# Performance work log

Hardware: AMD Instinct MI355X
Metric: run time of the kernel (lower is better)

## Reference

```python
import jax, jax.numpy as jnp
import numpy as np

PI = float(np.pi)


def _layernorm(x, g, b, eps=1e-5):
    mu = jnp.mean(x, axis=-1, keepdims=True)
    var = jnp.var(x, axis=-1, keepdims=True)
    return (x - mu) * jax.lax.rsqrt(var + eps) * g + b


def setup_inputs() -> dict:
    key = jax.random.key(0)
    B, L, D, P = 4, 2048, 256, 32
    ks = jax.random.split(key, 16)

    def lin_w(k, fi, fo):
        return (jax.random.normal(k, (fi, fo), dtype=jnp.float32) / np.sqrt(fi)).astype(jnp.float32)

    inp = {
        'x': jax.random.normal(ks[0], (B, L, D), dtype=jnp.float32),
        'pos_phases': jax.random.normal(ks[1], (L, P), dtype=jnp.float32) * PI,
        'w_mem1v': lin_w(ks[2], D, P), 'b_mem1v': jnp.zeros((P,), jnp.float32),
        'w_mem1o': lin_w(ks[3], P, D), 'b_mem1o': jnp.zeros((D,), jnp.float32),
        'w_off': lin_w(ks[4], D + P, P), 'b_off': jnp.zeros((P,), jnp.float32),
        'w_key': lin_w(ks[5], D, P), 'b_key': jnp.zeros((P,), jnp.float32),
        'w_val': lin_w(ks[6], D, D), 'b_val': jnp.zeros((D,), jnp.float32),
        'w_sk1': lin_w(ks[7], 2 * D, D), 'b_sk1': jnp.zeros((D,), jnp.float32),
        'w_sk2': lin_w(ks[8], D, P), 'b_sk2': jnp.zeros((P,), jnp.float32),
        'w_gate': lin_w(ks[9], D, 1), 'b_gate': jnp.zeros((1,), jnp.float32),
        'ln_g': jnp.ones((D,), jnp.float32), 'ln_b': jnp.zeros((D,), jnp.float32),
        'w_out': lin_w(ks[10], D, D), 'b_out': jnp.zeros((D,), jnp.float32),
    }
    return inp


def reference(x, pos_phases, w_mem1v, b_mem1v, w_mem1o, b_mem1o, w_off, b_off,
              w_key, b_key, w_val, b_val, w_sk1, b_sk1, w_sk2, b_sk2,
              w_gate, b_gate, ln_g, ln_b, w_out, b_out):
    B, L, D = x.shape
    P = pos_phases.shape[-1]

    pos_cos = jnp.cos(pos_phases)  # [L,P]
    pos_sin = jnp.sin(pos_phases)

    # Memory 1: flat [B,L,P] phasor cumulative memory
    v1 = x @ w_mem1v + b_mem1v                       # [B,L,P]
    mem1_cos = jnp.cumsum(pos_cos[None] * v1, axis=1)
    mem1_sin = jnp.cumsum(pos_sin[None] * v1, axis=1)

    offset_input = jnp.concatenate([x, jnp.broadcast_to(pos_phases[None], (B, L, P))], axis=-1)
    offset = jnp.tanh(offset_input @ w_off + b_off) * PI
    oc, os = jnp.cos(offset), jnp.sin(offset)
    query_cos = pos_cos[None] * oc - pos_sin[None] * os
    query_sin = pos_sin[None] * oc + pos_cos[None] * os
    pos_ret = (mem1_cos * query_cos + mem1_sin * query_sin) / np.sqrt(P)
    pos_out = pos_ret @ w_mem1o + b_mem1o            # [B,L,D]

    # Memory 2: full [B,L,P,D] phasor KV cumulative memory
    key_phases = jnp.tanh(x @ w_key + b_key) * PI    # [B,L,P]
    key_cos, key_sin = jnp.cos(key_phases), jnp.sin(key_phases)
    values = x @ w_val + b_val                       # [B,L,D]
    store_gate = jax.nn.sigmoid(x @ w_gate + b_gate) # [B,L,1]

    positions = jnp.arange(1, L + 1, dtype=x.dtype)[None, :, None]
    context_avg = jnp.cumsum(x, axis=1) / positions
    h = jax.nn.gelu(jnp.concatenate([x, context_avg], axis=-1) @ w_sk1 + b_sk1, approximate=False)
    storage_phases = jnp.tanh(h @ w_sk2 + b_sk2) * PI  # [B,L,P]

    gated_v = values * store_gate                    # [B,L,D]
    kv_mem_cos = jnp.cumsum(jnp.cos(storage_phases)[..., None] * gated_v[:, :, None, :], axis=1)  # [B,L,P,D]
    kv_mem_sin = jnp.cumsum(jnp.sin(storage_phases)[..., None] * gated_v[:, :, None, :], axis=1)

    gate_cumsum = jnp.clip(jnp.cumsum(store_gate, axis=1), 1.0, None)  # [B,L,1]
    kv_retrieved = jnp.einsum('blpd,blp->bld', kv_mem_cos, key_cos) + \
                   jnp.einsum('blpd,blp->bld', kv_mem_sin, key_sin)
    kv_retrieved = kv_retrieved / (jnp.sqrt(gate_cumsum) * np.sqrt(P))

    combined = pos_out + kv_retrieved
    return x + _layernorm(combined, ln_g, ln_b) @ w_out + b_out
```

## Files before the change

kernel.cpp:

```cpp
#include <hip/hip_runtime.h>
#include <hip/hip_bf16.h>

constexpr int B_ = 4;
constexpr int L_ = 2048;
constexpr int D_ = 256;
constexpr int P_ = 32;
constexpr int CL = 32;
constexpr int NC = L_ / CL;

#define PI_F 3.14159265358979323846f
#define INV_SQRT_P 0.17677669529663687f

typedef __attribute__((ext_vector_type(8))) short short8_t;
typedef __attribute__((ext_vector_type(4))) float floatx4;

static __device__ inline short f2bf(float f) {
  unsigned int u;
  __builtin_memcpy(&u, &f, 4);
  unsigned int r = (u + 0x7fffu + ((u >> 16) & 1u)) >> 16;
  return (short)r;
}
static __device__ inline float bf2f(short s) {
  unsigned int u = ((unsigned int)(unsigned short)s) << 16;
  float f;
  __builtin_memcpy(&f, &u, 4);
  return f;
}

__global__ void wprep(const float* __restrict__ x, const float* __restrict__ pos,
                      const float* __restrict__ w_val, const float* __restrict__ w_mem1v,
                      const float* __restrict__ w_off, const float* __restrict__ b_off,
                      const float* __restrict__ w_key, const float* __restrict__ w_gate,
                      const float* __restrict__ w_sk1, const float* __restrict__ w_out,
                      const float* __restrict__ w_sk2, const float* __restrict__ w_mem1o,
                      short* __restrict__ WA, short* __restrict__ W1,
                      short* __restrict__ WO, short* __restrict__ W2T,
                      short* __restrict__ W1OT,
                      short* __restrict__ xbf, float* __restrict__ poff,
                      float* __restrict__ ctxsum) {
  __shared__ float2 psum[2][128];
  int blk = blockIdx.x, tid = threadIdx.x;
  if (blk < 384) {
    int idx = blk * 256 + tid;
    int n = idx >> 8, k = idx & 255;
    float v;
    if (n < 256) v = w_val[k * 256 + n];
    else if (n < 288) v = w_mem1v[k * 32 + (n - 256)];
    else if (n < 320) v = w_off[k * 32 + (n - 288)];
    else if (n < 352) v = w_key[k * 32 + (n - 320)];
    else if (n == 352) v = w_gate[k];
    else v = 0.f;
    WA[idx] = f2bf(v);
  } else if (blk < 896) {
    int idx = (blk - 384) * 256 + tid;
    int n = idx >> 9, k = idx & 511;
    W1[idx] = f2bf(w_sk1[k * 256 + n]);
  } else if (blk < 1152) {
    int idx = (blk - 896) * 256 + tid;
    int n = idx >> 8, k = idx & 255;
    WO[idx] = f2bf(w_out[k * 256 + n]);
  } else if (blk < 1184) {
    int idx = (blk - 1152) * 256 + tid;
    int p = idx >> 8, k = idx & 255;
    W2T[idx] = f2bf(w_sk2[k * 32 + p]);
  } else if (blk < 1216) {
    int idx = (blk - 1184) * 256 + tid;
    int d = idx >> 5, p = idx & 31;
    W1OT[idx] = f2bf(w_mem1o[p * 256 + d]);
  } else if (blk < 1472) {
    int idx = (blk - 1216) * 256 + tid;
    int l = idx >> 5, p = idx & 31;
    float a = b_off[p];
#pragma unroll 8
    for (int j = 0; j < 32; ++j) a += pos[l * 32 + j] * w_off[(256 + j) * 32 + p];
    poff[idx] = a;
  } else {
    int c2 = blk - 1472;
    int b = c2 >> 6, ch = c2 & 63;
    int d2 = (tid & 127) * 2, h = tid >> 7;
    int tokb = b * L_ + ch * 32 + h * 16;
    float2 xv[16];
#pragma unroll
    for (int i = 0; i < 16; ++i)
      xv[i] = *(const float2*)&x[(tokb + i) * 256 + d2];
    float2 s = {0.f, 0.f};
#pragma unroll
    for (int i = 0; i < 16; ++i) { s.x += xv[i].x; s.y += xv[i].y; }
#pragma unroll
    for (int i = 0; i < 16; ++i) {
      short2 o;
      o.x = f2bf(xv[i].x);
      o.y = f2bf(xv[i].y);
      *(short2*)&xbf[(tokb + i) * 256 + d2] = o;
    }
    psum[h][tid & 127] = s;
    __syncthreads();
    if (h == 0) {
      float2 o = psum[1][tid & 127];
      float2 tot = {s.x + o.x, s.y + o.y};
      *(float2*)&ctxsum[c2 * 256 + d2] = tot;
    }
  }
}

__global__ __launch_bounds__(768, 6) void gemmA3(const short* __restrict__ xbf,
                                                 const short* __restrict__ WA,
                                                 const float* __restrict__ pos,
                                                 const float* __restrict__ poff,
                                                 const float* __restrict__ b_mem1v,
                                                 const float* __restrict__ b_key,
                                                 const float* __restrict__ b_gate,
                                                 const float* __restrict__ b_val,
                                                 float* __restrict__ m1cT,
                                                 float* __restrict__ m1sT,
                                                 float* __restrict__ qc,
                                                 float* __restrict__ qs,
                                                 short* __restrict__ K2bf,
                                                 short* __restrict__ gvT,
                                                 float* __restrict__ sg,
                                                 float* __restrict__ ctxsum) {
  __shared__ float YL[16][132];
  __shared__ float gsh[16];
  int tid = threadIdx.x;
  int bc = blockIdx.x;
  if (bc >= 512) {
    if (tid < 256) {
      int b = bc - 512;
      int base = b * 64 * 256 + tid;
      float run = 0.f;
      for (int c0 = 0; c0 < 64; c0 += 8) {
        float v[8];
#pragma unroll
        for (int j = 0; j < 8; ++j) v[j] = ctxsum[base + (c0 + j) * 256];
#pragma unroll
        for (int j = 0; j < 8; ++j) {
          ctxsum[base + (c0 + j) * 256] = run;
          run += v[j];
        }
      }
    }
    return;
  }
  int lane = tid & 63, w = tid >> 6;
  int ml = lane & 15, quad = lane >> 4, kq = quad * 8;
  int bc32 = bc >> 1, half = bc & 1;
  int tok0 = bc * 16;
  float posv = 0.f, poffv = 0.f;
  if (tid < 512) {
    int t = tid >> 5, p = tid & 31;
    int l = (tok0 + t) & (L_ - 1);
    posv = pos[l * 32 + p];
    poffv = poff[l * 32 + p];
  }
  floatx4 acc[2] = {};
  const short* A0p = &xbf[(tok0 + ml) * 256 + kq];
  const short* Bp = &WA[(w * 32 + ml) * 256 + kq];
#pragma unroll
  for (int ks = 0; ks < 8; ++ks) {
    short8_t a0 = *(const short8_t*)(A0p + ks * 32);
#pragma unroll
    for (int nt = 0; nt < 2; ++nt) {
      short8_t b = *(const short8_t*)(Bp + nt * 16 * 256 + ks * 32);
      acc[nt] = __builtin_amdgcn_mfma_f32_16x16x32_bf16(a0, b, acc[nt], 0, 0, 0);
    }
  }
  if (w >= 8) {
#pragma unroll
    for (int nt = 0; nt < 2; ++nt) {
      int col = (w - 8) * 32 + nt * 16 + ml;
#pragma unroll
      for (int r = 0; r < 4; ++r)
        YL[quad * 4 + r][col] = acc[nt][r];
    }
  }
  __syncthreads();
  if (tid < 512) {
    int t = tid >> 5, p = tid & 31;
    int tok = tok0 + t, l = tok & (L_ - 1);
    int b = tok >> 11;
    float v1 = YL[t][p] + b_mem1v[p];
    float pc = cosf(posv), ps = sinf(posv);
    int idxT = (b * 32 + p) * L_ + l;
    m1cT[idxT] = pc * v1;
    m1sT[idxT] = ps * v1;
    float off = tanhf(YL[t][32 + p] + poffv) * PI_F;
    float oc = cosf(off), os = sinf(off);
    int gidx = tok * 32 + p;
    qc[gidx] = pc * oc - ps * os;
    qs[gidx] = ps * oc + pc * os;
    float kp = tanhf(YL[t][64 + p] + b_key[p]) * PI_F;
    K2bf[tok * 64 + p] = f2bf(cosf(kp));
    K2bf[tok * 64 + 32 + p] = f2bf(sinf(kp));
    if (p == 0) {
      float g = 1.f / (1.f + expf(-(YL[t][96] + b_gate[0])));
      sg[tok] = g;
      gsh[t] = g;
    }
  }
  __syncthreads();
  if (w < 8) {
#pragma unroll
    for (int nt = 0; nt < 2; ++nt) {
      int d = w * 32 + nt * 16 + ml;
      float bv = b_val[d];
      int t0 = quad * 4;
      short4 o;
      o.x = f2bf((acc[nt][0] + bv) * gsh[t0 + 0]);
      o.y = f2bf((acc[nt][1] + bv) * gsh[t0 + 1]);
      o.z = f2bf((acc[nt][2] + bv) * gsh[t0 + 2]);
      o.w = f2bf((acc[nt][3] + bv) * gsh[t0 + 3]);
      *(short4*)&gvT[(bc32 * 256 + d) * 32 + half * 16 + t0] = o;
    }
  }
}

union __align__(16) CDMem {
  short As[32][520];
  struct { short HS[32][280]; short SPL[64][40]; } h;
};
__global__ __launch_bounds__(1024, 4) void gemmCD(const short* __restrict__ xbf,
                                                  const float* __restrict__ x,
                                                  const float* __restrict__ ctxsum,
                                                  const short* __restrict__ W1,
                                                  const float* __restrict__ b_sk1,
                                                  const short* __restrict__ W2T,
                                                  const float* __restrict__ b_sk2,
                                                  const short* __restrict__ gvT,
                                                  short* __restrict__ SPbf,
                                                  short* __restrict__ UT) {
  __shared__ CDMem sm;
  __shared__ float stmp[4][256];
  int tid = threadIdx.x;
  int bc = blockIdx.x;
  int tok0 = bc * 32;
  int bI = bc >> 6, ch = bc & 63;
  int lane = tid & 63, w = tid >> 6;
  int ml = lane & 15, quad = lane >> 4, kq = quad * 8;
  short8_t bgv = *(const short8_t*)&gvT[(bc * 256 + w * 16 + ml) * 32 + kq];
  {
    int row = tid >> 5, c8 = tid & 31;
    *(short8_t*)&sm.As[row][c8 * 8] =
        *(const short8_t*)&xbf[(tok0 + row) * 256 + c8 * 8];
  }
  {
    int d = tid & 255, qh = tid >> 8;
    float cp = ctxsum[(bI * 64 + ch) * 256 + d];
    float xv[8];
    int xb = (tok0 + qh * 8) * 256 + d;
#pragma unroll
    for (int i = 0; i < 8; ++i) xv[i] = x[xb + i * 256];
    float p = 0.f;
#pragma unroll
    for (int i = 0; i < 8; ++i) p += xv[i];
    stmp[qh][d] = p;
    __syncthreads();
    float run = cp;
    for (int j = 0; j < qh; ++j) run += stmp[j][d];
    int l0 = ch * 32 + qh * 8;
#pragma unroll
    for (int i = 0; i < 8; ++i) {
      run += xv[i];
      sm.As[qh * 8 + i][256 + d] = f2bf(run / (float)(l0 + i + 1));
    }
  }
  __syncthreads();
  int n0w = w * 16;
  floatx4 acc[2] = {};
#pragma unroll
  for (int kt = 0; kt < 16; ++kt) {
    short8_t a0 = *(short8_t*)&sm.As[ml][kt * 32 + kq];
    short8_t a1 = *(short8_t*)&sm.As[16 + ml][kt * 32 + kq];
    short8_t b0 = *(const short8_t*)&W1[(n0w + ml) * 512 + kt * 32 + kq];
    acc[0] = __builtin_amdgcn_mfma_f32_16x16x32_bf16(a0, b0, acc[0], 0, 0, 0);
    acc[1] = __builtin_amdgcn_mfma_f32_16x16x32_bf16(a1, b0, acc[1], 0, 0, 0);
  }
  short hv[2][4];
  {
    float bv = b_sk1[n0w + ml];
#pragma unroll
    for (int mt = 0; mt < 2; ++mt)
#pragma unroll
      for (int r = 0; r < 4; ++r) {
        float v = acc[mt][r] + bv;
        float g = 0.5f * v * (1.f + erff(v * 0.70710678118654752f));
        hv[mt][r] = f2bf(g);
      }
  }
  __syncthreads();
#pragma unroll
  for (int mt = 0; mt < 2; ++mt)
#pragma unroll
    for (int r = 0; r < 4; ++r)
      sm.h.HS[mt * 16 + quad * 4 + r][n0w + ml] = hv[mt][r];
  __syncthreads();
  if (w < 4) {
    int th = w & 1, ph = w >> 1;
    floatx4 pacc = {};
#pragma unroll
    for (int s = 0; s < 8; ++s) {
      short8_t a = *(short8_t*)&sm.h.HS[th * 16 + ml][s * 32 + kq];
      short8_t b0 = *(const short8_t*)&W2T[(ph * 16 + ml) * 256 + s * 32 + kq];
      pacc = __builtin_amdgcn_mfma_f32_16x16x32_bf16(a, b0, pacc, 0, 0, 0);
    }
    int p = ph * 16 + ml;
    float bs = b_sk2[p];
#pragma unroll
    for (int r = 0; r < 4; ++r) {
      int tl = th * 16 + quad * 4 + r;
      int tok = tok0 + tl;
      float sp = tanhf(pacc[r] + bs) * PI_F;
      short c = f2bf(cosf(sp)), s2 = f2bf(sinf(sp));
      sm.h.SPL[p][tl] = c;
      sm.h.SPL[32 + p][tl] = s2;
      SPbf[tok * 64 + p] = c;
      SPbf[tok * 64 + 32 + p] = s2;
    }
  }
  __syncthreads();
  short8_t a[4];
#pragma unroll
  for (int mt = 0; mt < 4; ++mt) a[mt] = *(short8_t*)&sm.h.SPL[mt * 16 + ml][kq];
  floatx4 acc3[4] = {};
#pragma unroll
  for (int mt = 0; mt < 4; ++mt)
    acc3[mt] = __builtin_amdgcn_mfma_f32_16x16x32_bf16(a[mt], bgv, acc3[mt], 0, 0, 0);
#pragma unroll
  for (int mt = 0; mt < 4; ++mt) {
    int d = w * 16 + ml;
    short4 o;
    o.x = f2bf(acc3[mt][0]);
    o.y = f2bf(acc3[mt][1]);
    o.z = f2bf(acc3[mt][2]);
    o.w = f2bf(acc3[mt][3]);
    *(short4*)&UT[(bc * 256 + d) * 64 + mt * 16 + quad * 4] = o;
  }
}

__global__ void scanE(float* __restrict__ m1cT, float* __restrict__ m1sT,
                      float* __restrict__ sg, short* __restrict__ UT) {
  __shared__ float wsum[4];
  __shared__ float stot[4][64];
  int blk = blockIdx.x;
  int tid = threadIdx.x;
  if (blk >= 260) {
    int eb = blk - 260;
    int w = tid >> 6, lane = tid & 63;
    int pi = eb * 64 + lane;
    int q = pi & 63;
    int d = (pi >> 6) & 255;
    int b = pi >> 14;
    const int cs = 256 * 64;
    int base = ((b * NC) * 256 + d) * 64 + q;
    short v[16];
#pragma unroll
    for (int c = 0; c < 16; ++c) v[c] = UT[base + (w * 16 + c) * cs];
    float tot = 0.f;
#pragma unroll
    for (int c = 0; c < 16; ++c) tot += bf2f(v[c]);
    stot[w][lane] = tot;
    __syncthreads();
    float run = 0.f;
    for (int ww = 0; ww < w; ++ww) run += stot[ww][lane];
#pragma unroll
    for (int c = 0; c < 16; ++c) {
      UT[base + (w * 16 + c) * cs] = f2bf(run);
      run += bf2f(v[c]);
    }
    return;
  }
  int lane = tid & 63, w = tid >> 6;
  float* arr;
  int base;
  if (blk < 256) {
    arr = (blk < 128) ? m1cT : m1sT;
    base = (blk & 127) * L_;
  } else {
    arr = sg;
    base = (blk - 256) * L_;
  }
  int sbase = base + w * 512;
  float v[8];
#pragma unroll
  for (int i = 0; i < 8; ++i) v[i] = arr[sbase + i * 64 + lane];
  float carry = 0.f;
#pragma unroll
  for (int i = 0; i < 8; ++i) {
    float vv = v[i];
#pragma unroll
    for (int off = 1; off < 64; off <<= 1) {
      float n = __shfl_up(vv, off, 64);
      if (lane >= off) vv += n;
    }
    vv += carry;
    v[i] = vv;
    carry = __shfl(vv, 63, 64);
  }
  if (lane == 0) wsum[w] = carry;
  __syncthreads();
  float off = 0.f;
  for (int ww = 0; ww < w; ++ww) off += wsum[ww];
#pragma unroll
  for (int i = 0; i < 8; ++i) arr[sbase + i * 64 + lane] = v[i] + off;
}

struct __align__(16) FGMem {
  short SL[32][40];
  short PR[32][40];
  float CMB[32][260];
  short CBN[32][280];
  float LG[256], LB[256];
  float scl[32], mu_s[32], rs_s[32];
};
__global__ __launch_bounds__(1024, 4) void fgOut(const short* __restrict__ UT,
                                                 const short* __restrict__ SPbf,
                                                 const short* __restrict__ K2bf,
                                                 const short* __restrict__ gvT,
                                                 const float* __restrict__ sgc,
                                                 const float* __restrict__ m1cT,
                                                 const float* __restrict__ m1sT,
                                                 const float* __restrict__ qc,
                                                 const float* __restrict__ qs,
                                                 const short* __restrict__ W1OT,
                                                 const float* __restrict__ b_mem1o,
                                                 const float* __restrict__ ln_g,
                                                 const float* __restrict__ ln_b,
                                                 const short* __restrict__ WO,
                                                 const float* __restrict__ b_out,
                                                 const float* __restrict__ x,
                                                 float* __restrict__ out) {
  __shared__ FGMem sm;
  int tid5 = threadIdx.x;
  int bc = blockIdx.x;
  int lbase = bc * CL;
  int bb = bc >> 6, lloc = (bc & 63) * 32;
  int lane = tid5 & 63, w = tid5 >> 6;
  int ml = lane & 15, quad = lane >> 4, kq = quad * 8;
  int d0 = w * 16;
  short8_t ub0 = *(const short8_t*)&UT[(bc * 256 + d0 + ml) * 64 + kq];
  short8_t ub1 = *(const short8_t*)&UT[(bc * 256 + d0 + ml) * 64 + 32 + kq];
  short8_t gvb = *(const short8_t*)&gvT[(bc * 256 + d0 + ml) * 32 + kq];
  short8_t w1b = *(const short8_t*)&W1OT[(d0 + ml) * 32 + kq];
  const float4* x4 = (const float4*)&x[lbase * 256];
  float4 xp0 = x4[tid5];
  float4 xp1 = x4[tid5 + 1024];
  if (tid5 < 32) sm.scl[tid5] = rsqrtf(fmaxf(sgc[lbase + tid5], 1.f)) * INV_SQRT_P;
  if (tid5 >= 256 && tid5 < 512) {
    int d = tid5 - 256;
    sm.LG[d] = ln_g[d];
    sm.LB[d] = ln_b[d];
  }
  short8_t ka0 = *(const short8_t*)&K2bf[(lbase + ml) * 64 + kq];
  short8_t ka1 = *(const short8_t*)&K2bf[(lbase + 16 + ml) * 64 + kq];
  short8_t kb0 = *(const short8_t*)&K2bf[(lbase + ml) * 64 + 32 + kq];
  short8_t kb1 = *(const short8_t*)&K2bf[(lbase + 16 + ml) * 64 + 32 + kq];
  if (w == 0) {
    floatx4 sacc[2][2] = {};
#pragma unroll
    for (int ks2 = 0; ks2 < 2; ++ks2) {
      short8_t a0 = (ks2 == 0) ? ka0 : kb0;
      short8_t a1 = (ks2 == 0) ? ka1 : kb1;
      short8_t b0 = *(const short8_t*)&SPbf[(lbase + ml) * 64 + ks2 * 32 + kq];
      short8_t b1 = *(const short8_t*)&SPbf[(lbase + 16 + ml) * 64 + ks2 * 32 + kq];
      sacc[0][0] = __builtin_amdgcn_mfma_f32_16x16x32_bf16(a0, b0, sacc[0][0], 0, 0, 0);
      sacc[0][1] = __builtin_amdgcn_mfma_f32_16x16x32_bf16(a0, b1, sacc[0][1], 0, 0, 0);
      sacc[1][0] = __builtin_amdgcn_mfma_f32_16x16x32_bf16(a1, b0, sacc[1][0], 0, 0, 0);
      sacc[1][1] = __builtin_amdgcn_mfma_f32_16x16x32_bf16(a1, b1, sacc[1][1], 0, 0, 0);
    }
#pragma unroll
    for (int mt = 0; mt < 2; ++mt)
#pragma unroll
      for (int nt = 0; nt < 2; ++nt)
#pragma unroll
        for (int r = 0; r < 4; ++r) {
          int trow = mt * 16 + quad * 4 + r;
          int scol = nt * 16 + ml;
          float v = (scol <= trow) ? sacc[mt][nt][r] : 0.f;
          sm.SL[trow][scol] = f2bf(v);
        }
  } else {
    int t7 = tid5 - 64;
    for (int i = t7; i < 1024; i += 960) {
      int pp = i >> 5, t = i & 31;
      int gT = (bb * 32 + pp) * L_ + lloc + t;
      int g = (lbase + t) * 32 + pp;
      sm.PR[t][pp] = f2bf((m1cT[gT] * qc[g] + m1sT[gT] * qs[g]) * INV_SQRT_P);
    }
  }
  __syncthreads();
  floatx4 acc[2] = {};
  acc[0] = __builtin_amdgcn_mfma_f32_16x16x32_bf16(ka0, ub0, acc[0], 0, 0, 0);
  acc[1] = __builtin_amdgcn_mfma_f32_16x16x32_bf16(ka1, ub0, acc[1], 0, 0, 0);
  acc[0] = __builtin_amdgcn_mfma_f32_16x16x32_bf16(kb0, ub1, acc[0], 0, 0, 0);
  acc[1] = __builtin_amdgcn_mfma_f32_16x16x32_bf16(kb1, ub1, acc[1], 0, 0, 0);
  {
    short8_t a0 = *(short8_t*)&sm.SL[ml][kq];
    short8_t a1 = *(short8_t*)&sm.SL[16 + ml][kq];
    acc[0] = __builtin_amdgcn_mfma_f32_16x16x32_bf16(a0, gvb, acc[0], 0, 0, 0);
    acc[1] = __builtin_amdgcn_mfma_f32_16x16x32_bf16(a1, gvb, acc[1], 0, 0, 0);
  }
  floatx4 macc[2] = {};
  {
    short8_t a0 = *(short8_t*)&sm.PR[ml][kq];
    short8_t a1 = *(short8_t*)&sm.PR[16 + ml][kq];
    macc[0] = __builtin_amdgcn_mfma_f32_16x16x32_bf16(a0, w1b, macc[0], 0, 0, 0);
    macc[1] = __builtin_amdgcn_mfma_f32_16x16x32_bf16(a1, w1b, macc[1], 0, 0, 0);
  }
  {
    int d = d0 + ml;
    float bm = b_mem1o[d];
#pragma unroll
    for (int mt = 0; mt < 2; ++mt)
#pragma unroll
      for (int r = 0; r < 4; ++r) {
        int t = mt * 16 + quad * 4 + r;
        sm.CMB[t][d] = acc[mt][r] * sm.scl[t] + macc[mt][r] + bm;
      }
  }
  __syncthreads();
  {
    int t = tid5 >> 5, g = tid5 & 31;
    float s = 0.f, s2 = 0.f;
#pragma unroll
    for (int j = 0; j < 8; ++j) {
      float v = sm.CMB[t][g + j * 32];
      s += v;
      s2 += v * v;
    }
#pragma unroll
    for (int m = 1; m < 32; m <<= 1) {
      s += __shfl_xor(s, m, 64);
      s2 += __shfl_xor(s2, m, 64);
    }
    if (g == 0) {
      float mu = s / (float)D_;
      float var = s2 / (float)D_ - mu * mu;
      sm.mu_s[t] = mu;
      sm.rs_s[t] = rsqrtf(var + 1e-5f);
    }
  }
  __syncthreads();
#pragma unroll
  for (int it = 0; it < 8; ++it) {
    int i = it * 1024 + tid5;
    int t = i >> 8, d = i & 255;
    sm.CBN[t][d] = f2bf((sm.CMB[t][d] - sm.mu_s[t]) * sm.rs_s[t] * sm.LG[d] + sm.LB[d]);
  }
  __syncthreads();
  floatx4 acc2[2] = {};
#pragma unroll
  for (int kt = 0; kt < 8; ++kt) {
    short8_t a0 = *(short8_t*)&sm.CBN[ml][kt * 32 + kq];
    short8_t a1 = *(short8_t*)&sm.CBN[16 + ml][kt * 32 + kq];
    short8_t b = *(const short8_t*)&WO[(d0 + ml) * 256 + kt * 32 + kq];
    acc2[0] = __builtin_amdgcn_mfma_f32_16x16x32_bf16(a0, b, acc2[0], 0, 0, 0);
    acc2[1] = __builtin_amdgcn_mfma_f32_16x16x32_bf16(a1, b, acc2[1], 0, 0, 0);
  }
  {
    int n = d0 + ml;
    float bv = b_out[n];
#pragma unroll
    for (int mt = 0; mt < 2; ++mt)
#pragma unroll
      for (int r = 0; r < 4; ++r) {
        int t = mt * 16 + quad * 4 + r;
        sm.CMB[t][n] = acc2[mt][r] + bv;
      }
  }
  __syncthreads();
  {
    float4* o4 = (float4*)&out[lbase * 256];
#pragma unroll
    for (int k = 0; k < 2; ++k) {
      int idx4 = tid5 + k * 1024;
      int t = idx4 >> 6, dd = (idx4 & 63) * 4;
      float4 xp = (k == 0) ? xp0 : xp1;
      float4 o;
      o.x = xp.x + sm.CMB[t][dd + 0];
      o.y = xp.y + sm.CMB[t][dd + 1];
      o.z = xp.z + sm.CMB[t][dd + 2];
      o.w = xp.w + sm.CMB[t][dd + 3];
      o4[idx4] = o;
    }
  }
}

extern "C" void kernel_launch(void* const* d_in, const int* in_sizes, int n_in,
                              void* d_out, int out_size, void* d_ws, size_t ws_size,
                              hipStream_t stream) {
  const float* x = (const float*)d_in[0];
  const float* pos = (const float*)d_in[1];
  const float* w_mem1v = (const float*)d_in[2];
  const float* b_mem1v = (const float*)d_in[3];
  const float* w_mem1o = (const float*)d_in[4];
  const float* b_mem1o = (const float*)d_in[5];
  const float* w_off = (const float*)d_in[6];
  const float* b_off = (const float*)d_in[7];
  const float* w_key = (const float*)d_in[8];
  const float* b_key = (const float*)d_in[9];
  const float* w_val = (const float*)d_in[10];
  const float* b_val = (const float*)d_in[11];
  const float* w_sk1 = (const float*)d_in[12];
  const float* b_sk1 = (const float*)d_in[13];
  const float* w_sk2 = (const float*)d_in[14];
  const float* b_sk2 = (const float*)d_in[15];
  const float* w_gate = (const float*)d_in[16];
  const float* b_gate = (const float*)d_in[17];
  const float* ln_g = (const float*)d_in[18];
  const float* ln_b = (const float*)d_in[19];
  const float* w_out = (const float*)d_in[20];
  const float* b_out = (const float*)d_in[21];
  float* out = (float*)d_out;
  float* ws = (float*)d_ws;

  const int BLP = B_ * L_ * P_;
  const int BLD = B_ * L_ * D_;
  float* m1cT = ws;
  float* m1sT = m1cT + BLP;
  float* qc = m1sT + BLP;
  float* qs = qc + BLP;
  float* sg = qs + BLP;
  float* poff = sg + B_ * L_;
  float* ctxsum = poff + L_ * P_;
  short* UT = (short*)(ctxsum + B_ * 64 * 256);
  short* xbf = UT + (size_t)B_ * NC * 256 * 64;
  short* ctxbf = xbf + BLD;
  short* hs = ctxbf + BLD;
  short* gvT = hs + BLD;
  short* K2bf = gvT + BLD;
  short* SPbf = K2bf + B_ * L_ * 64;
  short* WA = SPbf + B_ * L_ * 64;
  short* W1 = WA + 384 * 256;
  short* WO = W1 + 256 * 512;
  short* W2T = WO + 256 * 256;
  short* W1OT = W2T + 32 * 256;

  wprep<<<1728, 256, 0, stream>>>(x, pos, w_val, w_mem1v, w_off, b_off, w_key, w_gate,
                                  w_sk1, w_out, w_sk2, w_mem1o, WA, W1, WO, W2T, W1OT,
                                  xbf, poff, ctxsum);
  gemmA3<<<516, 768, 0, stream>>>(xbf, WA, pos, poff, b_mem1v, b_key, b_gate, b_val,
                                  m1cT, m1sT, qc, qs, K2bf, gvT, sg, ctxsum);
  gemmCD<<<256, 1024, 0, stream>>>(xbf, x, ctxsum, W1, b_sk1, W2T, b_sk2, gvT, SPbf, UT);
  scanE<<<1284, 256, 0, stream>>>(m1cT, m1sT, sg, UT);
  fgOut<<<256, 1024, 0, stream>>>(UT, SPbf, K2bf, gvT, sg, m1cT, m1sT, qc, qs,
                                  W1OT, b_mem1o, ln_g, ln_b, WO, b_out, x, out);
}
```

Measured before the change: 160.7 us.

## Split gemmCD and fgOut into two 512-thread blocks per chunk

gemmCD now launches two 512-thread blocks per 32-token chunk. Each block recomputes the shared sk1/sk2 stage redundantly, and the final value-projection output is split across the d halves. fgOut is split by token halves (16 tokens per block) with 32 output columns per wave. The aim is to double the number of blocks on the 256-CU part so the GPU is filled better, at the cost of redundant GEMM work in gemmCD and repeated loads in fgOut.

```diff
diff --git a/kernel.cpp b/kernel.cpp
--- a/kernel.cpp
+++ b/kernel.cpp
@@ -218,80 +218,89 @@
   short As[32][520];
   struct { short HS[32][280]; short SPL[64][40]; } h;
 };
-__global__ __launch_bounds__(1024, 4) void gemmCD(const short* __restrict__ xbf,
-                                                  const float* __restrict__ x,
-                                                  const float* __restrict__ ctxsum,
-                                                  const short* __restrict__ W1,
-                                                  const float* __restrict__ b_sk1,
-                                                  const short* __restrict__ W2T,
-                                                  const float* __restrict__ b_sk2,
-                                                  const short* __restrict__ gvT,
-                                                  short* __restrict__ SPbf,
-                                                  short* __restrict__ UT) {
+__global__ __launch_bounds__(512, 4) void gemmCD(const short* __restrict__ xbf,
+                                                 const float* __restrict__ x,
+                                                 const float* __restrict__ ctxsum,
+                                                 const short* __restrict__ W1,
+                                                 const float* __restrict__ b_sk1,
+                                                 const short* __restrict__ W2T,
+                                                 const float* __restrict__ b_sk2,
+                                                 const short* __restrict__ gvT,
+                                                 short* __restrict__ SPbf,
+                                                 short* __restrict__ UT) {
   __shared__ CDMem sm;
-  __shared__ float stmp[4][256];
+  __shared__ float stmp[256];
   int tid = threadIdx.x;
-  int bc = blockIdx.x;
-  int tok0 = bc * 32;
-  int bI = bc >> 6, ch = bc & 63;
+  int cn = blockIdx.x >> 1, dh = blockIdx.x & 1;
+  int tok0 = cn * 32;
+  int bI = cn >> 6, ch = cn & 63;
   int lane = tid & 63, w = tid >> 6;
   int ml = lane & 15, quad = lane >> 4, kq = quad * 8;
-  short8_t bgv = *(const short8_t*)&gvT[(bc * 256 + w * 16 + ml) * 32 + kq];
-  {
-    int row = tid >> 5, c8 = tid & 31;
+  short8_t bgv = *(const short8_t*)&gvT[(cn * 256 + dh * 128 + w * 16 + ml) * 32 + kq];
+#pragma unroll
+  for (int pass = 0; pass < 2; ++pass) {
+    int idx = pass * 512 + tid;
+    int row = idx >> 5, c8 = idx & 31;
     *(short8_t*)&sm.As[row][c8 * 8] =
         *(const short8_t*)&xbf[(tok0 + row) * 256 + c8 * 8];
   }
   {
     int d = tid & 255, qh = tid >> 8;
     float cp = ctxsum[(bI * 64 + ch) * 256 + d];
-    float xv[8];
-    int xb = (tok0 + qh * 8) * 256 + d;
-#pragma unroll
-    for (int i = 0; i < 8; ++i) xv[i] = x[xb + i * 256];
-    float p = 0.f;
-#pragma unroll
-    for (int i = 0; i < 8; ++i) p += xv[i];
-    stmp[qh][d] = p;
+    float xv[16];
+    int xb = (tok0 + qh * 16) * 256 + d;
+#pragma unroll
+    for (int i = 0; i < 16; ++i) xv[i] = x[xb + i * 256];
+    if (qh == 0) {
+      float p = 0.f;
+#pragma unroll
+      for (int i = 0; i < 16; ++i) p += xv[i];
+      stmp[d] = p;
+    }
     __syncthreads();
-    float run = cp;
-    for (int j = 0; j < qh; ++j) run += stmp[j][d];
-    int l0 = ch * 32 + qh * 8;
-#pragma unroll
-    for (int i = 0; i < 8; ++i) {
+    float run = cp + (qh ? stmp[d] : 0.f);
+    int l0 = ch * 32 + qh * 16;
+#pragma unroll
+    for (int i = 0; i < 16; ++i) {
       run += xv[i];
-      sm.As[qh * 8 + i][256 + d] = f2bf(run / (float)(l0 + i + 1));
-    }
-  }
-  __syncthreads();
-  int n0w = w * 16;
-  floatx4 acc[2] = {};
+      sm.As[qh * 16 + i][256 + d] = f2bf(run / (float)(l0 + i + 1));
+    }
+  }
+  __syncthreads();
+  int n0w = w * 32;
+  floatx4 acc[2][2] = {};
 #pragma unroll
   for (int kt = 0; kt < 16; ++kt) {
     short8_t a0 = *(short8_t*)&sm.As[ml][kt * 32 + kq];
     short8_t a1 = *(short8_t*)&sm.As[16 + ml][kt * 32 + kq];
     short8_t b0 = *(const short8_t*)&W1[(n0w + ml) * 512 + kt * 32 + kq];
-    acc[0] = __builtin_amdgcn_mfma_f32_16x16x32_bf16(a0, b0, acc[0], 0, 0, 0);
-    acc[1] = __builtin_amdgcn_mfma_f32_16x16x32_bf16(a1, b0, acc[1], 0, 0, 0);
-  }
-  short hv[2][4];
-  {
-    float bv = b_sk1[n0w + ml];
+    short8_t b1 = *(const short8_t*)&W1[(n0w + 16 + ml) * 512 + kt * 32 + kq];
+    acc[0][0] = __builtin_amdgcn_mfma_f32_16x16x32_bf16(a0, b0, acc[0][0], 0, 0, 0);
+    acc[0][1] = __builtin_amdgcn_mfma_f32_16x16x32_bf16(a0, b1, acc[0][1], 0, 0, 0);
+    acc[1][0] = __builtin_amdgcn_mfma_f32_16x16x32_bf16(a1, b0, acc[1][0], 0, 0, 0);
+    acc[1][1] = __builtin_amdgcn_mfma_f32_16x16x32_bf16(a1, b1, acc[1][1], 0, 0, 0);
+  }
+  short hv[2][2][4];
+#pragma unroll
+  for (int nt = 0; nt < 2; ++nt) {
+    float bv = b_sk1[n0w + nt * 16 + ml];
 #pragma unroll
     for (int mt = 0; mt < 2; ++mt)
 #pragma unroll
       for (int r = 0; r < 4; ++r) {
-        float v = acc[mt][r] + bv;
+        float v = acc[mt][nt][r] + bv;
         float g = 0.5f * v * (1.f + erff(v * 0.70710678118654752f));
-        hv[mt][r] = f2bf(g);
+        hv[mt][nt][r] = f2bf(g);
       }
   }
   __syncthreads();
 #pragma unroll
   for (int mt = 0; mt < 2; ++mt)
 #pragma unroll
-    for (int r = 0; r < 4; ++r)
-      sm.h.HS[mt * 16 + quad * 4 + r][n0w + ml] = hv[mt][r];
+    for (int nt = 0; nt < 2; ++nt)
+#pragma unroll
+      for (int r = 0; r < 4; ++r)
+        sm.h.HS[mt * 16 + quad * 4 + r][n0w + nt * 16 + ml] = hv[mt][nt][r];
   __syncthreads();
   if (w < 4) {
     int th = w & 1, ph = w >> 1;
@@ -312,8 +321,10 @@
       short c = f2bf(cosf(sp)), s2 = f2bf(sinf(sp));
       sm.h.SPL[p][tl] = c;
       sm.h.SPL[32 + p][tl] = s2;
-      SPbf[tok * 64 + p] = c;
-      SPbf[tok * 64 + 32 + p] = s2;
+      if (dh == 0) {
+        SPbf[tok * 64 + p] = c;
+        SPbf[tok * 64 + 32 + p] = s2;
+      }
     }
   }
   __syncthreads();
@@ -324,15 +335,17 @@
 #pragma unroll
   for (int mt = 0; mt < 4; ++mt)
     acc3[mt] = __builtin_amdgcn_mfma_f32_16x16x32_bf16(a[mt], bgv, acc3[mt], 0, 0, 0);
-#pragma unroll
-  for (int mt = 0; mt < 4; ++mt) {
-    int d = w * 16 + ml;
-    short4 o;
-    o.x = f2bf(acc3[mt][0]);
-    o.y = f2bf(acc3[mt][1]);
-    o.z = f2bf(acc3[mt][2]);
-    o.w = f2bf(acc3[mt][3]);
-    *(short4*)&UT[(bc * 256 + d) * 64 + mt * 16 + quad * 4] = o;
+  {
+    int d = dh * 128 + w * 16 + ml;
+#pragma unroll
+    for (int mt = 0; mt < 4; ++mt) {
+      short4 o;
+      o.x = f2bf(acc3[mt][0]);
+      o.y = f2bf(acc3[mt][1]);
+      o.z = f2bf(acc3[mt][2]);
+      o.w = f2bf(acc3[mt][3]);
+      *(short4*)&UT[(cn * 256 + d) * 64 + mt * 16 + quad * 4] = o;
+    }
   }
 }
 
@@ -404,125 +417,124 @@
 }
 
 struct __align__(16) FGMem {
-  short SL[32][40];
-  short PR[32][40];
-  float CMB[32][260];
-  short CBN[32][280];
+  short SL[16][40];
+  short PR[16][40];
+  float CMB[16][260];
+  short CBN[16][280];
   float LG[256], LB[256];
-  float scl[32], mu_s[32], rs_s[32];
+  float scl[16], mu_s[16], rs_s[16];
 };
-__global__ __launch_bounds__(1024, 4) void fgOut(const short* __restrict__ UT,
-                                                 const short* __restrict__ SPbf,
-                                                 const short* __restrict__ K2bf,
-                                                 const short* __restrict__ gvT,
-                                                 const float* __restrict__ sgc,
-                                                 const float* __restrict__ m1cT,
-                                                 const float* __restrict__ m1sT,
-                                                 const float* __restrict__ qc,
-                                                 const float* __restrict__ qs,
-                                                 const short* __restrict__ W1OT,
-                                                 const float* __restrict__ b_mem1o,
-                                                 const float* __restrict__ ln_g,
-                                                 const float* __restrict__ ln_b,
-                                                 const short* __restrict__ WO,
-                                                 const float* __restrict__ b_out,
-                                                 const float* __restrict__ x,
-                                                 float* __restrict__ out) {
+__global__ __launch_bounds__(512, 4) void fgOut(const short* __restrict__ UT,
+                                                const short* __restrict__ SPbf,
+                                                const short* __restrict__ K2bf,
+                                                const short* __restrict__ gvT,
+                                                const float* __restrict__ sgc,
+                                                const float* __restrict__ m1cT,
+                                                const float* __restrict__ m1sT,
+                                                const float* __restrict__ qc,
+                                                const float* __restrict__ qs,
+                                                const short* __restrict__ W1OT,
+                                                const float* __restrict__ b_mem1o,
+                                                const float* __restrict__ ln_g,
+                                                const float* __restrict__ ln_b,
+                                                const short* __restrict__ WO,
+                                                const float* __restrict__ b_out,
+                                                const float* __restrict__ x,
+                                                float* __restrict__ out) {
   __shared__ FGMem sm;
-  int tid5 = threadIdx.x;
-  int bc = blockIdx.x;
-  int lbase = bc * CL;
-  int bb = bc >> 6, lloc = (bc & 63) * 32;
-  int lane = tid5 & 63, w = tid5 >> 6;
+  int tid = threadIdx.x;
+  int cn = blockIdx.x >> 1, th = blockIdx.x & 1;
+  int lbase = cn * CL;
+  int tb = lbase + th * 16;
+  int bb = cn >> 6, lloc = (cn & 63) * 32;
+  int lane = tid & 63, w = tid >> 6;
   int ml = lane & 15, quad = lane >> 4, kq = quad * 8;
-  int d0 = w * 16;
-  short8_t ub0 = *(const short8_t*)&UT[(bc * 256 + d0 + ml) * 64 + kq];
-  short8_t ub1 = *(const short8_t*)&UT[(bc * 256 + d0 + ml) * 64 + 32 + kq];
-  short8_t gvb = *(const short8_t*)&gvT[(bc * 256 + d0 + ml) * 32 + kq];
-  short8_t w1b = *(const short8_t*)&W1OT[(d0 + ml) * 32 + kq];
-  const float4* x4 = (const float4*)&x[lbase * 256];
-  float4 xp0 = x4[tid5];
-  float4 xp1 = x4[tid5 + 1024];
-  if (tid5 < 32) sm.scl[tid5] = rsqrtf(fmaxf(sgc[lbase + tid5], 1.f)) * INV_SQRT_P;
-  if (tid5 >= 256 && tid5 < 512) {
-    int d = tid5 - 256;
+  int d0 = w * 32;
+  short8_t ub[2][2], gvb[2], w1b[2];
+#pragma unroll
+  for (int nt = 0; nt < 2; ++nt) {
+    int d = d0 + nt * 16 + ml;
+    ub[nt][0] = *(const short8_t*)&UT[(cn * 256 + d) * 64 + kq];
+    ub[nt][1] = *(const short8_t*)&UT[(cn * 256 + d) * 64 + 32 + kq];
+    gvb[nt] = *(const short8_t*)&gvT[(cn * 256 + d) * 32 + kq];
+    w1b[nt] = *(const short8_t*)&W1OT[d * 32 + kq];
+  }
+  const float4* x4 = (const float4*)&x[tb * 256];
+  float4 xp0 = x4[tid];
+  float4 xp1 = x4[tid + 512];
+  if (tid < 16) sm.scl[tid] = rsqrtf(fmaxf(sgc[tb + tid], 1.f)) * INV_SQRT_P;
+  if (tid >= 256) {
+    int d = tid - 256;
     sm.LG[d] = ln_g[d];
     sm.LB[d] = ln_b[d];
   }
-  short8_t ka0 = *(const short8_t*)&K2bf[(lbase + ml) * 64 + kq];
-  short8_t ka1 = *(const short8_t*)&K2bf[(lbase + 16 + ml) * 64 + kq];
-  short8_t kb0 = *(const short8_t*)&K2bf[(lbase + ml) * 64 + 32 + kq];
-  short8_t kb1 = *(const short8_t*)&K2bf[(lbase + 16 + ml) * 64 + 32 + kq];
+  short8_t ka0 = *(const short8_t*)&K2bf[(tb + ml) * 64 + kq];
+  short8_t kb0 = *(const short8_t*)&K2bf[(tb + ml) * 64 + 32 + kq];
   if (w == 0) {
-    floatx4 sacc[2][2] = {};
+    floatx4 sacc[2] = {};
 #pragma unroll
     for (int ks2 = 0; ks2 < 2; ++ks2) {
-      short8_t a0 = (ks2 == 0) ? ka0 : kb0;
-      short8_t a1 = (ks2 == 0) ? ka1 : kb1;
+      short8_t a = (ks2 == 0) ? ka0 : kb0;
       short8_t b0 = *(const short8_t*)&SPbf[(lbase + ml) * 64 + ks2 * 32 + kq];
       short8_t b1 = *(const short8_t*)&SPbf[(lbase + 16 + ml) * 64 + ks2 * 32 + kq];
-      sacc[0][0] = __builtin_amdgcn_mfma_f32_16x16x32_bf16(a0, b0, sacc[0][0], 0, 0, 0);
-      sacc[0][1] = __builtin_amdgcn_mfma_f32_16x16x32_bf16(a0, b1, sacc[0][1], 0, 0, 0);
-      sacc[1][0] = __builtin_amdgcn_mfma_f32_16x16x32_bf16(a1, b0, sacc[1][0], 0, 0, 0);
-      sacc[1][1] = __builtin_amdgcn_mfma_f32_16x16x32_bf16(a1, b1, sacc[1][1], 0, 0, 0);
-    }
-#pragma unroll
-    for (int mt = 0; mt < 2; ++mt)
-#pragma unroll
-      for (int nt = 0; nt < 2; ++nt)
-#pragma unroll
-        for (int r = 0; r < 4; ++r) {
-          int trow = mt * 16 + quad * 4 + r;
-          int scol = nt * 16 + ml;
-          float v = (scol <= trow) ? sacc[mt][nt][r] : 0.f;
-          sm.SL[trow][scol] = f2bf(v);
-        }
+      sacc[0] = __builtin_amdgcn_mfma_f32_16x16x32_bf16(a, b0, sacc[0], 0, 0, 0);
+      sacc[1] = __builtin_amdgcn_mfma_f32_16x16x32_bf16(a, b1, sacc[1], 0, 0, 0);
+    }
+#pragma unroll
+    for (int nt = 0; nt < 2; ++nt)
+#pragma unroll
+      for (int r = 0; r < 4; ++r) {
+        int trowL = quad * 4 + r;
+        int tl = th * 16 + trowL;
+        int scol = nt * 16 + ml;
+        float v = (scol <= tl) ? sacc[nt][r] : 0.f;
+        sm.SL[trowL][scol] = f2bf(v);
+      }
   } else {
-    int t7 = tid5 - 64;
-    for (int i = t7; i < 1024; i += 960) {
-      int pp = i >> 5, t = i & 31;
-      int gT = (bb * 32 + pp) * L_ + lloc + t;
-      int g = (lbase + t) * 32 + pp;
-      sm.PR[t][pp] = f2bf((m1cT[gT] * qc[g] + m1sT[gT] * qs[g]) * INV_SQRT_P);
+    for (int i = tid - 64; i < 512; i += 448) {
+      int pp = i >> 4, t16 = i & 15;
+      int gT = (bb * 32 + pp) * L_ + lloc + th * 16 + t16;
+      int g = (tb + t16) * 32 + pp;
+      sm.PR[t16][pp] = f2bf((m1cT[gT] * qc[g] + m1sT[gT] * qs[g]) * INV_SQRT_P);
     }
   }
   __syncthreads();
   floatx4 acc[2] = {};
-  acc[0] = __builtin_amdgcn_mfma_f32_16x16x32_bf16(ka0, ub0, acc[0], 0, 0, 0);
-  acc[1] = __builtin_amdgcn_mfma_f32_16x16x32_bf16(ka1, ub0, acc[1], 0, 0, 0);
-  acc[0] = __builtin_amdgcn_mfma_f32_16x16x32_bf16(kb0, ub1, acc[0], 0, 0, 0);
-  acc[1] = __builtin_amdgcn_mfma_f32_16x16x32_bf16(kb1, ub1, acc[1], 0, 0, 0);
+#pragma unroll
+  for (int nt = 0; nt < 2; ++nt) {
+    acc[nt] = __builtin_amdgcn_mfma_f32_16x16x32_bf16(ka0, ub[nt][0], acc[nt], 0, 0, 0);
+    acc[nt] = __builtin_amdgcn_mfma_f32_16x16x32_bf16(kb0, ub[nt][1], acc[nt], 0, 0, 0);
+  }
   {
     short8_t a0 = *(short8_t*)&sm.SL[ml][kq];
-    short8_t a1 = *(short8_t*)&sm.SL[16 + ml][kq];
-    acc[0] = __builtin_amdgcn_mfma_f32_16x16x32_bf16(a0, gvb, acc[0], 0, 0, 0);
-    acc[1] = __builtin_amdgcn_mfma_f32_16x16x32_bf16(a1, gvb, acc[1], 0, 0, 0);
+#pragma unroll
+    for (int nt = 0; nt < 2; ++nt)
+      acc[nt] = __builtin_amdgcn_mfma_f32_16x16x32_bf16(a0, gvb[nt], acc[nt], 0, 0, 0);
   }
   floatx4 macc[2] = {};
   {
     short8_t a0 = *(short8_t*)&sm.PR[ml][kq];
-    short8_t a1 = *(short8_t*)&sm.PR[16 + ml][kq];
-    macc[0] = __builtin_amdgcn_mfma_f32_16x16x32_bf16(a0, w1b, macc[0], 0, 0, 0);
-    macc[1] = __builtin_amdgcn_mfma_f32_16x16x32_bf16(a1, w1b, macc[1], 0, 0, 0);
-  }
+#pragma unroll
+    for (int nt = 0; nt < 2; ++nt)
+      macc[nt] = __builtin_amdgcn_mfma_f32_16x16x32_bf16(a0, w1b[nt], macc[nt], 0, 0, 0);
+  }
+#pragma unroll
+  for (int nt = 0; nt < 2; ++nt) {
+    int d = d0 + nt * 16 + ml;
+    float bm = b_mem1o[d];
+#pragma unroll
+    for (int r = 0; r < 4; ++r) {
+      int t16 = quad * 4 + r;
+      sm.CMB[t16][d] = acc[nt][r] * sm.scl[t16] + macc[nt][r] + bm;
+    }
+  }
+  __syncthreads();
   {
-    int d = d0 + ml;
-    float bm = b_mem1o[d];
-#pragma unroll
-    for (int mt = 0; mt < 2; ++mt)
-#pragma unroll
-      for (int r = 0; r < 4; ++r) {
-        int t = mt * 16 + quad * 4 + r;
-        sm.CMB[t][d] = acc[mt][r] * sm.scl[t] + macc[mt][r] + bm;
-      }
-  }
-  __syncthreads();
-  {
-    int t = tid5 >> 5, g = tid5 & 31;
+    int t16 = tid >> 5, g = tid & 31;
     float s = 0.f, s2 = 0.f;
 #pragma unroll
     for (int j = 0; j < 8; ++j) {
-      float v = sm.CMB[t][g + j * 32];
+      float v = sm.CMB[t16][g + j * 32];
       s += v;
       s2 += v * v;
     }
@@ -534,51 +546,51 @@
     if (g == 0) {
       float mu = s / (float)D_;
       float var = s2 / (float)D_ - mu * mu;
-      sm.mu_s[t] = mu;
-      sm.rs_s[t] = rsqrtf(var + 1e-5f);
+      sm.mu_s[t16] = mu;
+      sm.rs_s[t16] = rsqrtf(var + 1e-5f);
     }
   }
   __syncthreads();
 #pragma unroll
   for (int it = 0; it < 8; ++it) {
-    int i = it * 1024 + tid5;
-    int t = i >> 8, d = i & 255;
-    sm.CBN[t][d] = f2bf((sm.CMB[t][d] - sm.mu_s[t]) * sm.rs_s[t] * sm.LG[d] + sm.LB[d]);
+    int i = it * 512 + tid;
+    int t16 = i >> 8, d = i & 255;
+    sm.CBN[t16][d] = f2bf((sm.CMB[t16][d] - sm.mu_s[t16]) * sm.rs_s[t16] * sm.LG[d] + sm.LB[d]);
   }
   __syncthreads();
   floatx4 acc2[2] = {};
 #pragma unroll
   for (int kt = 0; kt < 8; ++kt) {
     short8_t a0 = *(short8_t*)&sm.CBN[ml][kt * 32 + kq];
-    short8_t a1 = *(short8_t*)&sm.CBN[16 + ml][kt * 32 + kq];
-    short8_t b = *(const short8_t*)&WO[(d0 + ml) * 256 + kt * 32 + kq];
-    acc2[0] = __builtin_amdgcn_mfma_f32_16x16x32_bf16(a0, b, acc2[0], 0, 0, 0);
-    acc2[1] = __builtin_amdgcn_mfma_f32_16x16x32_bf16(a1, b, acc2[1], 0, 0, 0);
-  }
+#pragma unroll
+    for (int nt = 0; nt < 2; ++nt) {
+      short8_t b = *(const short8_t*)&WO[(d0 + nt * 16 + ml) * 256 + kt * 32 + kq];
+      acc2[nt] = __builtin_amdgcn_mfma_f32_16x16x32_bf16(a0, b, acc2[nt], 0, 0, 0);
+    }
+  }
+#pragma unroll
+  for (int nt = 0; nt < 2; ++nt) {
+    int n = d0 + nt * 16 + ml;
+    float bv = b_out[n];
+#pragma unroll
+    for (int r = 0; r < 4; ++r) {
+      int t16 = quad * 4 + r;
+      sm.CMB[t16][n] = acc2[nt][r] + bv;
+    }
+  }
+  __syncthreads();
   {
-    int n = d0 + ml;
-    float bv = b_out[n];
-#pragma unroll
-    for (int mt = 0; mt < 2; ++mt)
-#pragma unroll
-      for (int r = 0; r < 4; ++r) {
-        int t = mt * 16 + quad * 4 + r;
-        sm.CMB[t][n] = acc2[mt][r] + bv;
-      }
-  }
-  __syncthreads();
-  {
-    float4* o4 = (float4*)&out[lbase * 256];
+    float4* o4 = (float4*)&out[tb * 256];
 #pragma unroll
     for (int k = 0; k < 2; ++k) {
-      int idx4 = tid5 + k * 1024;
-      int t = idx4 >> 6, dd = (idx4 & 63) * 4;
+      int idx4 = tid + k * 512;
+      int t16 = idx4 >> 6, dd = (idx4 & 63) * 4;
       float4 xp = (k == 0) ? xp0 : xp1;
       float4 o;
-      o.x = xp.x + sm.CMB[t][dd + 0];
-      o.y = xp.y + sm.CMB[t][dd + 1];
-      o.z = xp.z + sm.CMB[t][dd + 2];
-      o.w = xp.w + sm.CMB[t][dd + 3];
+      o.x = xp.x + sm.CMB[t16][dd + 0];
+      o.y = xp.y + sm.CMB[t16][dd + 1];
+      o.z = xp.z + sm.CMB[t16][dd + 2];
+      o.w = xp.w + sm.CMB[t16][dd + 3];
       o4[idx4] = o;
     }
   }
@@ -639,8 +651,8 @@
                                   xbf, poff, ctxsum);
   gemmA3<<<516, 768, 0, stream>>>(xbf, WA, pos, poff, b_mem1v, b_key, b_gate, b_val,
                                   m1cT, m1sT, qc, qs, K2bf, gvT, sg, ctxsum);
-  gemmCD<<<256, 1024, 0, stream>>>(xbf, x, ctxsum, W1, b_sk1, W2T, b_sk2, gvT, SPbf, UT);
+  gemmCD<<<512, 512, 0, stream>>>(xbf, x, ctxsum, W1, b_sk1, W2T, b_sk2, gvT, SPbf, UT);
   scanE<<<1284, 256, 0, stream>>>(m1cT, m1sT, sg, UT);
-  fgOut<<<256, 1024, 0, stream>>>(UT, SPbf, K2bf, gvT, sg, m1cT, m1sT, qc, qs,
-                                  W1OT, b_mem1o, ln_g, ln_b, WO, b_out, x, out);
-}
+  fgOut<<<512, 512, 0, stream>>>(UT, SPbf, K2bf, gvT, sg, m1cT, m1sT, qc, qs,
+                                 W1OT, b_mem1o, ln_g, ln_b, WO, b_out, x, out);
+}
```

Result: slower. 173.0 us (+7.7%).
